# Optimization experiments

Hardware: AMD Instinct MI355X
Metric: run time of the kernel (lower is better)

The kernel has to match this reference:

```python
import jax, jax.numpy as jnp
import numpy as np
import math

D_MODEL = 512
SLOPE = 0.5  # slope_init, not trainable


def setup_inputs() -> dict:
    key = jax.random.key(0)
    k1, k2, k3, k4 = jax.random.split(key, 4)
    B, S, D = 4, 4096, D_MODEL
    x = jax.random.normal(k1, (B, S, D), dtype=jnp.float32)
    # nn.Linear(d, d): weight is [d, d]; query_key weight used as x @ W (no transpose, bias unused)
    lim = 1.0 / math.sqrt(D)
    W_qk = jax.random.uniform(k2, (D, D), jnp.float32, -lim, lim)
    W_v = jax.random.uniform(k3, (D, D), jnp.float32, -lim, lim)
    b_v = jax.random.uniform(k4, (D,), jnp.float32, -lim, lim)
    return {"x": x, "W_qk": W_qk, "W_v": W_v, "b_v": b_v}


def reference(x, W_qk, W_v, b_v):
    B, S, D = x.shape
    scale = 1.0 / math.sqrt(D)
    # scores[b,i,j] = (x @ W_qk @ x^T) * scale   (torch: x @ weight @ x.transpose)
    scores = jnp.einsum('bid,de,bje->bij', x, W_qk, x) * scale
    # ALiBi bias: (j - i) * slope
    i = jnp.arange(S, dtype=x.dtype)[:, None]
    j = jnp.arange(S, dtype=x.dtype)[None, :]
    scores = scores + (j - i) * jnp.asarray(SLOPE, x.dtype)
    # causal mask: strict upper triangle -> -inf
    causal = j > i  # [S, S] bool
    scores = jnp.where(causal, -jnp.inf, scores)
    attn = jax.nn.softmax(scores, axis=-1)
    # value_linear: x @ W_v^T + b_v (standard nn.Linear)
    v = jnp.einsum('bjd,ed->bje', x, W_v) + b_v
    return jnp.einsum('bij,bje->bie', attn, v)
```

## Files before the change

### kernel.cpp

```cpp
#include <hip/hip_runtime.h>
#include <math.h>

#define D_MODEL 512
#define SEQ     4096
#define BATCH   4
#define BS      (BATCH * SEQ)

typedef __attribute__((ext_vector_type(8))) short  short8;
typedef __attribute__((ext_vector_type(4))) float  float4v;

#define GAS __attribute__((address_space(1)))
#define LAS __attribute__((address_space(3)))

__device__ __forceinline__ void gld_lds16(const void* g, void* l) {
  __builtin_amdgcn_global_load_lds((const GAS unsigned int*)g,
                                   (LAS unsigned int*)l, 16, 0, 0);
}

__device__ __forceinline__ unsigned short bf16r(float f) {
  unsigned int u = __builtin_bit_cast(unsigned int, f);
  u += 0x7fffu + ((u >> 16) & 1u);
  return (unsigned short)(u >> 16);
}

__device__ __forceinline__ uint4 pack8(float4 a, float4 b) {
  uint4 o;
  o.x = bf16r(a.x) | ((unsigned)bf16r(a.y) << 16);
  o.y = bf16r(a.z) | ((unsigned)bf16r(a.w) << 16);
  o.z = bf16r(b.x) | ((unsigned)bf16r(b.y) << 16);
  o.w = bf16r(b.z) | ((unsigned)bf16r(b.w) << 16);
  return o;
}

__global__ __launch_bounds__(256) void cvt_w(const float* __restrict__ Wqk,
                                             unsigned short* __restrict__ Wqkt,
                                             const float* __restrict__ Wv,
                                             unsigned short* __restrict__ Wvb,
                                             const float* __restrict__ x,
                                             unsigned short* __restrict__ xb) {
  if (blockIdx.x < 64) {
    __shared__ float tile[64][65];
    const int bx = blockIdx.x & 7;
    const int by = blockIdx.x >> 3;
    const int tx = threadIdx.x & 63;
    const int ty = threadIdx.x >> 6;
    for (int r = ty; r < 64; r += 4)
      tile[r][tx] = Wqk[(size_t)(by * 64 + r) * D_MODEL + bx * 64 + tx];
    __syncthreads();
    for (int r = ty; r < 64; r += 4)
      Wqkt[(size_t)(bx * 64 + r) * D_MODEL + by * 64 + tx] = bf16r(tile[tx][r]);
  } else if (blockIdx.x < 192) {
    const int idx = ((blockIdx.x - 64) * 256 + threadIdx.x) * 8;
    const float4 a = *(const float4*)(Wv + idx);
    const float4 b = *(const float4*)(Wv + idx + 4);
    *(uint4*)(Wvb + idx) = pack8(a, b);
  } else {
    const size_t idx = ((size_t)(blockIdx.x - 192) * 256 + threadIdx.x) * 8;
    const float4 a = *(const float4*)(x + idx);
    const float4 b = *(const float4*)(x + idx + 4);
    *(uint4*)(xb + idx) = pack8(a, b);
  }
}

__global__ __launch_bounds__(512, 1) void qv_gemm(const unsigned short* __restrict__ xb,
                                                  const unsigned short* __restrict__ Wqkt,
                                                  const unsigned short* __restrict__ Wvb,
                                                  const float* __restrict__ bv,
                                                  unsigned short* __restrict__ Qb,
                                                  unsigned short* __restrict__ Vt,
                                                  float scale) {
  __shared__ unsigned short As[2][256 * 64];
  __shared__ unsigned short Bs[2][256 * 64];

  const int t    = threadIdx.x;
  const int w    = t >> 6;
  const int lane = t & 63;
  const int q    = lane >> 4;
  const int c    = lane & 15;
  const int wr   = w >> 1;
  const int wc   = w & 1;
  const int sw   = c & 7;

  const int mt = blockIdx.x & 63;
  const int nt = blockIdx.x >> 6;
  const int a0 = mt * 256;
  const int b0 = (nt & 1) * 256;
  const bool vt = (nt >= 2);
  const unsigned short* __restrict__ Wgt = vt ? Wvb : Wqkt;

  float4v acc[4][8];
#pragma unroll
  for (int i = 0; i < 4; ++i)
#pragma unroll
    for (int j = 0; j < 8; ++j) acc[i][j] = (float4v){0.f, 0.f, 0.f, 0.f};

  auto stage = [&](int buf, int k0) {
#pragma unroll
    for (int it = 0; it < 4; ++it) {
      const int idx = it * 512 + t;
      const int r   = idx >> 3;
      const int ss  = idx & 7;
      const int ko  = k0 + ((ss ^ (r & 7)) << 3);
      gld_lds16(xb + (size_t)(a0 + r) * D_MODEL + ko, &As[buf][idx * 8]);
      gld_lds16(Wgt + (size_t)(b0 + r) * D_MODEL + ko, &Bs[buf][idx * 8]);
    }
  };

  stage(0, 0);
  __syncthreads();

  for (int slab = 0; slab < 8; ++slab) {
    const int buf = slab & 1;
    if (slab < 7) stage(buf ^ 1, (slab + 1) * 64);

    const unsigned short* SA = vt ? Bs[buf] : As[buf];
    const unsigned short* SB = vt ? As[buf] : Bs[buf];

#pragma unroll
    for (int kc = 0; kc < 2; ++kc) {
      const int slot = ((kc * 4 + q) ^ sw) * 8;
      short8 af[4], bf[8];
#pragma unroll
      for (int i = 0; i < 4; ++i)
        af[i] = *(const short8*)&SA[(wr * 64 + i * 16 + c) * 64 + slot];
#pragma unroll
      for (int j = 0; j < 8; ++j)
        bf[j] = *(const short8*)&SB[(wc * 128 + j * 16 + c) * 64 + slot];
#pragma unroll
      for (int i = 0; i < 4; ++i)
#pragma unroll
        for (int j = 0; j < 8; ++j)
          acc[i][j] = __builtin_amdgcn_mfma_f32_16x16x32_bf16(af[i], bf[j], acc[i][j], 0, 0, 0);
    }
    __syncthreads();
  }

  if (!vt) {
#pragma unroll
    for (int i = 0; i < 4; ++i)
#pragma unroll
      for (int tt = 0; tt < 4; ++tt) {
        const int row = a0 + wr * 64 + i * 16 + 4 * q + tt;
        const int cb  = nt * 256 + wc * 128;
#pragma unroll
        for (int j = 0; j < 8; ++j)
          Qb[(size_t)row * D_MODEL + cb + j * 16 + c] = bf16r(scale * acc[i][j][tt]);
      }
  } else {
#pragma unroll
    for (int i = 0; i < 4; ++i)
#pragma unroll
      for (int tt = 0; tt < 4; ++tt) {
        const int dim = (nt - 2) * 256 + wr * 64 + i * 16 + 4 * q + tt;
        const float bvv = bv[dim];
        const int kb  = a0 + wc * 128;
#pragma unroll
        for (int j = 0; j < 8; ++j)
          Vt[(size_t)dim * BS + kb + j * 16 + c] = bf16r(acc[i][j][tt] + bvv);
      }
  }
}

__global__ __launch_bounds__(128) void attn_tile(const unsigned short* __restrict__ Q,
                                                 const unsigned short* __restrict__ Kx,
                                                 const unsigned short* __restrict__ Vt,
                                                 float* __restrict__ out) {
  constexpr int PLD = 72;
  __shared__ unsigned short pls[16 * PLD];
  __shared__ float lm[2][16], ls[2][16];

  const int t    = threadIdx.x;
  const int h    = t >> 6;
  const int lane = t & 63;
  const int q    = lane >> 4;
  const int c    = lane & 15;

  const int tile = ((blockIdx.x & 7) << 7) + (blockIdx.x >> 3);
  const int r0   = tile << 4;
  const int b    = r0 >> 12;
  const int i0   = r0 & (SEQ - 1);
  const int jb   = i0 - 48;

  short8 qf[16];
  {
    const unsigned short* qp = Q + (size_t)(r0 + c) * D_MODEL + q * 8;
#pragma unroll
    for (int ch = 0; ch < 16; ++ch) qf[ch] = *(const short8*)(qp + ch * 32);
  }

  float4v sacc[2];
  sacc[0] = (float4v){0.f, 0.f, 0.f, 0.f};
  sacc[1] = (float4v){0.f, 0.f, 0.f, 0.f};
#pragma unroll
  for (int s = 0; s < 2; ++s) {
    const int sj = 2 * h + s;
    if (jb + 16 * sj + 15 < 0) continue;
    int krow = jb + 16 * sj + c;
    if (krow < 0) krow = 0;
    const unsigned short* kr = Kx + ((size_t)(b << 12) + krow) * D_MODEL + q * 8;
    float4v sv = sacc[s];
#pragma unroll
    for (int ch = 0; ch < 16; ++ch)
      sv = __builtin_amdgcn_mfma_f32_16x16x32_bf16(qf[ch], *(const short8*)(kr + ch * 32), sv, 0, 0, 0);
    sacc[s] = sv;
  }

  const unsigned short* vbase = Vt + (size_t)(h * 256 + c) * BS + (b << 12);
  const bool ch0 = (jb + 31 >= 0);
  short8 vf0[16];
  if (ch0) {
    int kk = jb + q * 8;
    if (kk < 0) kk = 0;
    const unsigned short* vb = vbase + kk;
#pragma unroll
    for (int dt = 0; dt < 16; ++dt) vf0[dt] = *(const short8*)(vb + (size_t)dt * 16 * BS);
  }

  float tmax[4] = {-1e30f, -1e30f, -1e30f, -1e30f};
#pragma unroll
  for (int s = 0; s < 2; ++s)
#pragma unroll
    for (int tt = 0; tt < 4; ++tt) {
      const int jl = jb + 16 * (2 * h + s) + c;
      const int il = i0 + 4 * q + tt;
      float sv = sacc[s][tt];
      sv = (jl < 0 || jl > il) ? -1e30f : sv + 0.5f * (float)(jl - il);
      sacc[s][tt] = sv;
      tmax[tt] = fmaxf(tmax[tt], sv);
    }
#pragma unroll
  for (int tt = 0; tt < 4; ++tt) {
    float v = tmax[tt];
    v = fmaxf(v, __shfl_xor(v, 1, 64));
    v = fmaxf(v, __shfl_xor(v, 2, 64));
    v = fmaxf(v, __shfl_xor(v, 4, 64));
    v = fmaxf(v, __shfl_xor(v, 8, 64));
    tmax[tt] = v;
  }
  if (c == 0) {
#pragma unroll
    for (int tt = 0; tt < 4; ++tt) lm[h][4 * q + tt] = tmax[tt];
  }
  __syncthreads();

  float m[4];
#pragma unroll
  for (int tt = 0; tt < 4; ++tt)
    m[tt] = fmaxf(lm[0][4 * q + tt], lm[1][4 * q + tt]);

  float rsum[4] = {0.f, 0.f, 0.f, 0.f};
#pragma unroll
  for (int s = 0; s < 2; ++s)
#pragma unroll
    for (int tt = 0; tt < 4; ++tt) {
      const float p = __expf(sacc[s][tt] - m[tt]);
      rsum[tt] += p;
      pls[(4 * q + tt) * PLD + (2 * h + s) * 16 + c] = bf16r(p);
    }
#pragma unroll
  for (int tt = 0; tt < 4; ++tt) {
    float v = rsum[tt];
    v += __shfl_xor(v, 1, 64);
    v += __shfl_xor(v, 2, 64);
    v += __shfl_xor(v, 4, 64);
    v += __shfl_xor(v, 8, 64);
    rsum[tt] = v;
  }
  if (c == 0) {
#pragma unroll
    for (int tt = 0; tt < 4; ++tt) ls[h][4 * q + tt] = rsum[tt];
  }
  __syncthreads();

  float l[4];
#pragma unroll
  for (int tt = 0; tt < 4; ++tt)
    l[tt] = ls[0][4 * q + tt] + ls[1][4 * q + tt];

  float4v oacc[16];
#pragma unroll
  for (int dt = 0; dt < 16; ++dt) oacc[dt] = (float4v){0.f, 0.f, 0.f, 0.f};

  if (ch0) {
    const short8 pa = *(const short8*)&pls[c * PLD + q * 8];
#pragma unroll
    for (int dt = 0; dt < 16; ++dt)
      oacc[dt] = __builtin_amdgcn_mfma_f32_16x16x32_bf16(pa, vf0[dt], oacc[dt], 0, 0, 0);
  }
  {
    const short8 pa = *(const short8*)&pls[c * PLD + 32 + q * 8];
    int kk = jb + 32 + q * 8;
    if (kk < 0) kk = 0;
    const unsigned short* vb = vbase + kk;
#pragma unroll
    for (int dt = 0; dt < 16; ++dt) {
      const short8 vf = *(const short8*)(vb + (size_t)dt * 16 * BS);
      oacc[dt] = __builtin_amdgcn_mfma_f32_16x16x32_bf16(pa, vf, oacc[dt], 0, 0, 0);
    }
  }

  float inv[4];
#pragma unroll
  for (int tt = 0; tt < 4; ++tt) inv[tt] = 1.0f / l[tt];
#pragma unroll
  for (int dt = 0; dt < 16; ++dt)
#pragma unroll
    for (int tt = 0; tt < 4; ++tt)
      out[(size_t)(r0 + 4 * q + tt) * D_MODEL + h * 256 + dt * 16 + c] =
          oacc[dt][tt] * inv[tt];
}

extern "C" void kernel_launch(void* const* d_in, const int* in_sizes, int n_in,
                              void* d_out, int out_size, void* d_ws,
                              size_t ws_size, hipStream_t stream) {
  const float* x   = (const float*)d_in[0];
  const float* Wqk = (const float*)d_in[1];
  const float* Wv  = (const float*)d_in[2];
  const float* bv  = (const float*)d_in[3];
  float* out = (float*)d_out;

  unsigned short* xb   = (unsigned short*)d_ws;
  unsigned short* Qb   = xb + (size_t)BS * D_MODEL;
  unsigned short* Vt   = Qb + (size_t)BS * D_MODEL;
  unsigned short* Wqkt = Vt + (size_t)BS * D_MODEL;
  unsigned short* Wvb  = Wqkt + (size_t)D_MODEL * D_MODEL;

  const float scale = 1.0f / sqrtf((float)D_MODEL);

  cvt_w<<<dim3(192 + (BS * D_MODEL / 2048)), dim3(256), 0, stream>>>(Wqk, Wqkt, Wv, Wvb, x, xb);
  qv_gemm<<<dim3(256), dim3(512), 0, stream>>>(xb, Wqkt, Wvb, bv, Qb, Vt, scale);
  attn_tile<<<dim3(BS / 16), dim3(128), 0, stream>>>(Qb, xb, Vt, out);
}
```

Before: 132.8 us.

## Shrink QV GEMM tiles to 128x128 with more blocks and packed stores

The projection GEMM moves from 256 blocks of 512 threads with 256x256 double-buffered tiles to 1024 blocks of 256 threads with 128x128 single-buffered tiles. Each wave's accumulator footprint shrinks and up to four blocks can share a CU. The goal is to fill all CUs, since 256 large blocks leave the 256-CU device with one block each and poor latency hiding. The epilogue now swaps operand roles so each lane writes four contiguous bf16 values as one 8-byte store instead of scattered 2-byte stores. In exchange, operand loads are no longer overlapped with compute inside a block, and smaller tiles give less reuse of global data.

```diff
diff --git a/kernel.cpp b/kernel.cpp
--- a/kernel.cpp
+++ b/kernel.cpp
@@ -62,15 +62,15 @@
   }
 }
 
-__global__ __launch_bounds__(512, 1) void qv_gemm(const unsigned short* __restrict__ xb,
+__global__ __launch_bounds__(256, 4) void qv_gemm(const unsigned short* __restrict__ xb,
                                                   const unsigned short* __restrict__ Wqkt,
                                                   const unsigned short* __restrict__ Wvb,
                                                   const float* __restrict__ bv,
                                                   unsigned short* __restrict__ Qb,
                                                   unsigned short* __restrict__ Vt,
                                                   float scale) {
-  __shared__ unsigned short As[2][256 * 64];
-  __shared__ unsigned short Bs[2][256 * 64];
+  __shared__ unsigned short As[128 * 64];
+  __shared__ unsigned short Bs[128 * 64];
 
   const int t    = threadIdx.x;
   const int w    = t >> 6;
@@ -81,55 +81,45 @@
   const int wc   = w & 1;
   const int sw   = c & 7;
 
-  const int mt = blockIdx.x & 63;
-  const int nt = blockIdx.x >> 6;
-  const int a0 = mt * 256;
-  const int b0 = (nt & 1) * 256;
-  const bool vt = (nt >= 2);
+  const int mt = blockIdx.x & 127;
+  const int nt = blockIdx.x >> 7;
+  const int a0 = mt * 128;
+  const bool vt = (nt >= 4);
+  const int b0 = (vt ? (nt - 4) : nt) * 128;
   const unsigned short* __restrict__ Wgt = vt ? Wvb : Wqkt;
 
-  float4v acc[4][8];
+  float4v acc[4][4];
 #pragma unroll
   for (int i = 0; i < 4; ++i)
 #pragma unroll
-    for (int j = 0; j < 8; ++j) acc[i][j] = (float4v){0.f, 0.f, 0.f, 0.f};
-
-  auto stage = [&](int buf, int k0) {
+    for (int j = 0; j < 4; ++j) acc[i][j] = (float4v){0.f, 0.f, 0.f, 0.f};
+
+  for (int k0 = 0; k0 < D_MODEL; k0 += 64) {
 #pragma unroll
     for (int it = 0; it < 4; ++it) {
-      const int idx = it * 512 + t;
+      const int idx = it * 256 + t;
       const int r   = idx >> 3;
-      const int ss  = idx & 7;
-      const int ko  = k0 + ((ss ^ (r & 7)) << 3);
-      gld_lds16(xb + (size_t)(a0 + r) * D_MODEL + ko, &As[buf][idx * 8]);
-      gld_lds16(Wgt + (size_t)(b0 + r) * D_MODEL + ko, &Bs[buf][idx * 8]);
-    }
-  };
-
-  stage(0, 0);
-  __syncthreads();
-
-  for (int slab = 0; slab < 8; ++slab) {
-    const int buf = slab & 1;
-    if (slab < 7) stage(buf ^ 1, (slab + 1) * 64);
-
-    const unsigned short* SA = vt ? Bs[buf] : As[buf];
-    const unsigned short* SB = vt ? As[buf] : Bs[buf];
+      const int s   = idx & 7;
+      const int ko  = k0 + ((s ^ (r & 7)) << 3);
+      gld_lds16(xb  + (size_t)(a0 + r) * D_MODEL + ko, &As[idx * 8]);
+      gld_lds16(Wgt + (size_t)(b0 + r) * D_MODEL + ko, &Bs[idx * 8]);
+    }
+    __syncthreads();
 
 #pragma unroll
     for (int kc = 0; kc < 2; ++kc) {
       const int slot = ((kc * 4 + q) ^ sw) * 8;
-      short8 af[4], bf[8];
+      short8 af[4], bf[4];
 #pragma unroll
       for (int i = 0; i < 4; ++i)
-        af[i] = *(const short8*)&SA[(wr * 64 + i * 16 + c) * 64 + slot];
-#pragma unroll
-      for (int j = 0; j < 8; ++j)
-        bf[j] = *(const short8*)&SB[(wc * 128 + j * 16 + c) * 64 + slot];
+        af[i] = *(const short8*)&(vt ? As : Bs)[(wr * 64 + i * 16 + c) * 64 + slot];
+#pragma unroll
+      for (int j = 0; j < 4; ++j)
+        bf[j] = *(const short8*)&(vt ? Bs : As)[(wc * 64 + j * 16 + c) * 64 + slot];
 #pragma unroll
       for (int i = 0; i < 4; ++i)
 #pragma unroll
-        for (int j = 0; j < 8; ++j)
+        for (int j = 0; j < 4; ++j)
           acc[i][j] = __builtin_amdgcn_mfma_f32_16x16x32_bf16(af[i], bf[j], acc[i][j], 0, 0, 0);
     }
     __syncthreads();
@@ -137,27 +127,34 @@
 
   if (!vt) {
 #pragma unroll
-    for (int i = 0; i < 4; ++i)
-#pragma unroll
-      for (int tt = 0; tt < 4; ++tt) {
-        const int row = a0 + wr * 64 + i * 16 + 4 * q + tt;
-        const int cb  = nt * 256 + wc * 128;
-#pragma unroll
-        for (int j = 0; j < 8; ++j)
-          Qb[(size_t)row * D_MODEL + cb + j * 16 + c] = bf16r(scale * acc[i][j][tt]);
+    for (int j = 0; j < 4; ++j) {
+      const size_t row = a0 + wc * 64 + j * 16 + c;
+#pragma unroll
+      for (int i = 0; i < 4; ++i) {
+        uint2 pkt;
+        pkt.x = (unsigned)bf16r(scale * acc[i][j][0]) |
+                ((unsigned)bf16r(scale * acc[i][j][1]) << 16);
+        pkt.y = (unsigned)bf16r(scale * acc[i][j][2]) |
+                ((unsigned)bf16r(scale * acc[i][j][3]) << 16);
+        *(uint2*)&Qb[row * D_MODEL + nt * 128 + wr * 64 + i * 16 + 4 * q] = pkt;
       }
+    }
   } else {
 #pragma unroll
-    for (int i = 0; i < 4; ++i)
-#pragma unroll
-      for (int tt = 0; tt < 4; ++tt) {
-        const int dim = (nt - 2) * 256 + wr * 64 + i * 16 + 4 * q + tt;
-        const float bvv = bv[dim];
-        const int kb  = a0 + wc * 128;
-#pragma unroll
-        for (int j = 0; j < 8; ++j)
-          Vt[(size_t)dim * BS + kb + j * 16 + c] = bf16r(acc[i][j][tt] + bvv);
+    for (int j = 0; j < 4; ++j) {
+      const int dim = (nt - 4) * 128 + wc * 64 + j * 16 + c;
+      const float bvv = bv[dim];
+#pragma unroll
+      for (int i = 0; i < 4; ++i) {
+        const int key = a0 + wr * 64 + i * 16 + 4 * q;
+        uint2 pkt;
+        pkt.x = (unsigned)bf16r(acc[i][j][0] + bvv) |
+                ((unsigned)bf16r(acc[i][j][1] + bvv) << 16);
+        pkt.y = (unsigned)bf16r(acc[i][j][2] + bvv) |
+                ((unsigned)bf16r(acc[i][j][3] + bvv) << 16);
+        *(uint2*)&Vt[(size_t)dim * BS + key] = pkt;
       }
+    }
   }
 }
 
@@ -328,6 +325,6 @@
   const float scale = 1.0f / sqrtf((float)D_MODEL);
 
   cvt_w<<<dim3(192 + (BS * D_MODEL / 2048)), dim3(256), 0, stream>>>(Wqk, Wqkt, Wv, Wvb, x, xb);
-  qv_gemm<<<dim3(256), dim3(512), 0, stream>>>(xb, Wqkt, Wvb, bv, Qb, Vt, scale);
+  qv_gemm<<<dim3(1024), dim3(256), 0, stream>>>(xb, Wqkt, Wvb, bv, Qb, Vt, scale);
   attn_tile<<<dim3(BS / 16), dim3(128), 0, stream>>>(Qb, xb, Vt, out);
 }
```

After: 132.2 us. About the same (-0.4%).

## Pre-swizzle x into a GEMM tile layout and deepen the load pipeline

Applied to the files above, without the earlier changes.

The convert kernel now writes x twice: a row-major bf16 copy for attention, and a second copy already blocked and XOR-swizzled into the GEMM's 256x64 LDS tile order. The QV GEMM can then stage A tiles with contiguous 16-byte loads. The GEMM main loop switches to explicit vmcnt waits and raw barriers so the next two slabs prefetch while the current one computes. It also swaps the operand roles so each thread's epilogue writes packed 4-element bf16 stores instead of scalar stores. The risks are that one thread per row in the convert kernel gives strided, poorly coalesced loads over only 64 blocks, and that launch_bounds(512,2) may force the 128-register accumulator to spill while LDS use still permits only one block per CU.

```diff
diff --git a/kernel.cpp b/kernel.cpp
--- a/kernel.cpp
+++ b/kernel.cpp
@@ -37,7 +37,8 @@
                                              const float* __restrict__ Wv,
                                              unsigned short* __restrict__ Wvb,
                                              const float* __restrict__ x,
-                                             unsigned short* __restrict__ xb) {
+                                             unsigned short* __restrict__ xb,
+                                             unsigned short* __restrict__ xbB) {
   if (blockIdx.x < 64) {
     __shared__ float tile[64][65];
     const int bx = blockIdx.x & 7;
@@ -55,14 +56,34 @@
     const float4 b = *(const float4*)(Wv + idx + 4);
     *(uint4*)(Wvb + idx) = pack8(a, b);
   } else {
-    const size_t idx = ((size_t)(blockIdx.x - 192) * 256 + threadIdx.x) * 8;
-    const float4 a = *(const float4*)(x + idx);
-    const float4 b = *(const float4*)(x + idx + 4);
-    *(uint4*)(xb + idx) = pack8(a, b);
-  }
-}
-
-__global__ __launch_bounds__(512, 1) void qv_gemm(const unsigned short* __restrict__ xb,
+    const int mt = blockIdx.x - 192;
+    const int r  = threadIdx.x;
+    const int row = mt * 256 + r;
+    const float* xr = x + (size_t)row * D_MODEL;
+    const int rk = r & 7;
+#pragma unroll 1
+    for (int slab = 0; slab < 8; ++slab) {
+      const int k0 = slab * 64;
+      float4 f[16];
+#pragma unroll
+      for (int i = 0; i < 16; ++i) f[i] = *(const float4*)(xr + k0 + i * 4);
+      uint4 lin[8];
+#pragma unroll
+      for (int s = 0; s < 8; ++s) lin[s] = pack8(f[s * 2], f[s * 2 + 1]);
+#pragma unroll
+      for (int s = 0; s < 8; ++s)
+        *(uint4*)&xb[(size_t)row * D_MODEL + k0 + s * 8] = lin[s];
+      unsigned short* bb = xbB + (((size_t)(mt * 8 + slab) * 2048) + r * 8) * 8;
+#pragma unroll
+      for (int s = 0; s < 8; ++s) {
+        const int cs = s ^ rk;
+        *(uint4*)&bb[s * 8] = lin[cs];
+      }
+    }
+  }
+}
+
+__global__ __launch_bounds__(512, 2) void qv_gemm(const unsigned short* __restrict__ xbB,
                                                   const unsigned short* __restrict__ Wqkt,
                                                   const unsigned short* __restrict__ Wvb,
                                                   const float* __restrict__ bv,
@@ -84,8 +105,8 @@
   const int mt = blockIdx.x & 63;
   const int nt = blockIdx.x >> 6;
   const int a0 = mt * 256;
+  const bool vt = (nt >= 2);
   const int b0 = (nt & 1) * 256;
-  const bool vt = (nt >= 2);
   const unsigned short* __restrict__ Wgt = vt ? Wvb : Wqkt;
 
   float4v acc[4][8];
@@ -94,27 +115,30 @@
 #pragma unroll
     for (int j = 0; j < 8; ++j) acc[i][j] = (float4v){0.f, 0.f, 0.f, 0.f};
 
-  auto stage = [&](int buf, int k0) {
+  auto stage = [&](int buf, int slab) {
+    const unsigned short* ab = xbB + (size_t)(mt * 8 + slab) * 16384;
+    const int k0 = slab * 64;
 #pragma unroll
     for (int it = 0; it < 4; ++it) {
       const int idx = it * 512 + t;
-      const int r   = idx >> 3;
-      const int ss  = idx & 7;
-      const int ko  = k0 + ((ss ^ (r & 7)) << 3);
-      gld_lds16(xb + (size_t)(a0 + r) * D_MODEL + ko, &As[buf][idx * 8]);
-      gld_lds16(Wgt + (size_t)(b0 + r) * D_MODEL + ko, &Bs[buf][idx * 8]);
+      gld_lds16(ab + idx * 8, &As[buf][idx * 8]);
+      const int r  = idx >> 3;
+      const int ss = idx & 7;
+      gld_lds16(Wgt + (size_t)(b0 + r) * D_MODEL + k0 + ((ss ^ (r & 7)) << 3),
+                &Bs[buf][idx * 8]);
     }
   };
 
   stage(0, 0);
-  __syncthreads();
-
-  for (int slab = 0; slab < 8; ++slab) {
-    const int buf = slab & 1;
-    if (slab < 7) stage(buf ^ 1, (slab + 1) * 64);
-
-    const unsigned short* SA = vt ? Bs[buf] : As[buf];
-    const unsigned short* SB = vt ? As[buf] : Bs[buf];
+  stage(1, 1);
+  asm volatile("s_waitcnt vmcnt(8)" ::: "memory");
+  asm volatile("s_barrier" ::: "memory");
+
+#pragma unroll 1
+  for (int s = 0; s < 8; ++s) {
+    const int cur = s & 1;
+    const unsigned short* SA = vt ? As[cur] : Bs[cur];
+    const unsigned short* SB = vt ? Bs[cur] : As[cur];
 
 #pragma unroll
     for (int kc = 0; kc < 2; ++kc) {
@@ -132,32 +156,46 @@
         for (int j = 0; j < 8; ++j)
           acc[i][j] = __builtin_amdgcn_mfma_f32_16x16x32_bf16(af[i], bf[j], acc[i][j], 0, 0, 0);
     }
-    __syncthreads();
+
+    asm volatile("s_barrier" ::: "memory");
+    if (s + 2 < 8) stage(cur, s + 2);
+    if (s + 1 < 8) {
+      if (s + 2 < 8) asm volatile("s_waitcnt vmcnt(8)" ::: "memory");
+      else           asm volatile("s_waitcnt vmcnt(0)" ::: "memory");
+      asm volatile("s_barrier" ::: "memory");
+    }
   }
 
   if (!vt) {
 #pragma unroll
-    for (int i = 0; i < 4; ++i)
-#pragma unroll
-      for (int tt = 0; tt < 4; ++tt) {
-        const int row = a0 + wr * 64 + i * 16 + 4 * q + tt;
-        const int cb  = nt * 256 + wc * 128;
-#pragma unroll
-        for (int j = 0; j < 8; ++j)
-          Qb[(size_t)row * D_MODEL + cb + j * 16 + c] = bf16r(scale * acc[i][j][tt]);
+    for (int j = 0; j < 8; ++j) {
+      const size_t row = a0 + wc * 128 + j * 16 + c;
+#pragma unroll
+      for (int i = 0; i < 4; ++i) {
+        uint2 pkt;
+        pkt.x = (unsigned)bf16r(scale * acc[i][j][0]) |
+                ((unsigned)bf16r(scale * acc[i][j][1]) << 16);
+        pkt.y = (unsigned)bf16r(scale * acc[i][j][2]) |
+                ((unsigned)bf16r(scale * acc[i][j][3]) << 16);
+        *(uint2*)&Qb[row * D_MODEL + nt * 256 + wr * 64 + i * 16 + 4 * q] = pkt;
       }
+    }
   } else {
 #pragma unroll
-    for (int i = 0; i < 4; ++i)
-#pragma unroll
-      for (int tt = 0; tt < 4; ++tt) {
-        const int dim = (nt - 2) * 256 + wr * 64 + i * 16 + 4 * q + tt;
-        const float bvv = bv[dim];
-        const int kb  = a0 + wc * 128;
-#pragma unroll
-        for (int j = 0; j < 8; ++j)
-          Vt[(size_t)dim * BS + kb + j * 16 + c] = bf16r(acc[i][j][tt] + bvv);
+    for (int j = 0; j < 8; ++j) {
+      const int dim = (nt - 2) * 256 + wc * 128 + j * 16 + c;
+      const float bvv = bv[dim];
+#pragma unroll
+      for (int i = 0; i < 4; ++i) {
+        const int key = a0 + wr * 64 + i * 16 + 4 * q;
+        uint2 pkt;
+        pkt.x = (unsigned)bf16r(acc[i][j][0] + bvv) |
+                ((unsigned)bf16r(acc[i][j][1] + bvv) << 16);
+        pkt.y = (unsigned)bf16r(acc[i][j][2] + bvv) |
+                ((unsigned)bf16r(acc[i][j][3] + bvv) << 16);
+        *(uint2*)&Vt[(size_t)dim * BS + key] = pkt;
       }
+    }
   }
 }
 
@@ -324,10 +362,11 @@
   unsigned short* Vt   = Qb + (size_t)BS * D_MODEL;
   unsigned short* Wqkt = Vt + (size_t)BS * D_MODEL;
   unsigned short* Wvb  = Wqkt + (size_t)D_MODEL * D_MODEL;
+  unsigned short* xbB  = Wvb + (size_t)D_MODEL * D_MODEL;
 
   const float scale = 1.0f / sqrtf((float)D_MODEL);
 
-  cvt_w<<<dim3(192 + (BS * D_MODEL / 2048)), dim3(256), 0, stream>>>(Wqk, Wqkt, Wv, Wvb, x, xb);
-  qv_gemm<<<dim3(256), dim3(512), 0, stream>>>(xb, Wqkt, Wvb, bv, Qb, Vt, scale);
+  cvt_w<<<dim3(256), dim3(256), 0, stream>>>(Wqk, Wqkt, Wv, Wvb, x, xb, xbB);
+  qv_gemm<<<dim3(256), dim3(512), 0, stream>>>(xbB, Wqkt, Wvb, bv, Qb, Vt, scale);
   attn_tile<<<dim3(BS / 16), dim3(128), 0, stream>>>(Qb, xb, Vt, out);
 }
```

Result: slower. 208.8 us (+57.2%).
